# Kernel optimization log

Hardware: AMD Instinct MI355X
Metric: run time of the kernel (lower is better)

## Reference

```python
import jax, jax.numpy as jnp
import numpy as np

T, A, H, E = 16, 8, 128, 32  # steps, actions/step, hidden, embed


def setup_inputs() -> dict:
    key = jax.random.key(0)
    ks = jax.random.split(key, 16)
    n = lambda k, s: jax.random.normal(k, s, dtype=jnp.float32) * 0.1
    return {
        "old_actions": jax.random.randint(ks[0], (T,), 0, A),
        "init_input": n(ks[1], (1, E)),
        "W_ih_a": n(ks[2], (4 * H, E)), "W_hh_a": n(ks[3], (4 * H, H)),
        "b_ih_a": n(ks[4], (4 * H,)), "b_hh_a": n(ks[5], (4 * H,)),
        "heads_W": n(ks[6], (T, A, H)), "heads_b": n(ks[7], (T, A)),
        "W_ih_c": n(ks[8], (4 * H, E)), "W_hh_c": n(ks[9], (4 * H, H)),
        "b_ih_c": n(ks[10], (4 * H,)), "b_hh_c": n(ks[11], (4 * H,)),
        "critic_W": n(ks[12], (1, H)), "critic_b": n(ks[13], (1,)),
        "embed": n(ks[14], (T * A, E)),
    }


def _lstm_cell(x, h, c, W_ih, W_hh, b_ih, b_hh):
    # PyTorch LSTMCell: gate order i, f, g, o
    g = W_ih @ x + b_ih + W_hh @ h + b_hh
    i, f, gg, o = jnp.split(g, 4)
    c = jax.nn.sigmoid(f) * c + jax.nn.sigmoid(i) * jnp.tanh(gg)
    h = jax.nn.sigmoid(o) * jnp.tanh(c)
    return h, c


def reference(old_actions, init_input, W_ih_a, W_hh_a, b_ih_a, b_hh_a,
              heads_W, heads_b, W_ih_c, W_hh_c, b_ih_c, b_hh_c,
              critic_W, critic_b, embed):
    # input sequence is fully determined by the given actions
    global_idx = jnp.arange(T) * A + old_actions          # action offsets
    emb_rows = embed[global_idx]                          # [T, E]
    x_seq = jnp.concatenate([init_input, emb_rows[:-1]], axis=0)  # [T, E]

    def step(carry, xs):
        h_a, c_a, h_c, c_c = carry
        x, hw, hb, a = xs
        h_a, c_a = _lstm_cell(x, h_a, c_a, W_ih_a, W_hh_a, b_ih_a, b_hh_a)
        logits = hw @ h_a + hb                            # [A]
        logp = jax.nn.log_softmax(logits)
        probs = jnp.exp(logp)
        lp = logp[a]
        ent = -jnp.sum(probs * logp)
        h_c, c_c = _lstm_cell(x, h_c, c_c, W_ih_c, W_hh_c, b_ih_c, b_hh_c)
        val = critic_W[0] @ h_c + critic_b[0]
        return (h_a, c_a, h_c, c_c), (lp, ent, val)

    z = jnp.zeros((H,), jnp.float32)
    _, (log_probs, entropies, values) = jax.lax.scan(
        step, (z, z, z, z), (x_seq, heads_W, heads_b, old_actions))
    return log_probs, entropies, values  # each [T]
```

## Files before the change

kernel.cpp:

```cpp
#include <hip/hip_runtime.h>
#include <math.h>

#define T 16
#define A 8
#define H 128
#define E 32
#define G (4*H)

#define WS_WHH(L)   ((size_t)(L) * 131072u)
#define WS_ACCX(L)  (262144u + (size_t)(L) * 32768u)

typedef _Float16 h2t __attribute__((ext_vector_type(2)));
typedef _Float16 h8t __attribute__((ext_vector_type(8)));

__device__ __forceinline__ float sigmoidf_(float x) {
    return 1.0f / (1.0f + __expf(-x));
}
__device__ __forceinline__ float tanhf_(float x) {
    return 1.0f - 2.0f / (1.0f + __expf(2.0f * x));
}

#if __has_builtin(__builtin_amdgcn_fdot2)
#define DOT2(a, b, c) __builtin_amdgcn_fdot2((a), (b), (c), false)
#else
__device__ __forceinline__ float dot2_fb(h2t a, h2t b, float c) {
    return fmaf((float)a[0], (float)b[0], fmaf((float)a[1], (float)b[1], c));
}
#define DOT2(a, b, c) dot2_fb((a), (b), (c))
#endif

#define RPT16(M) M(0) M(1) M(2) M(3) M(4) M(5) M(6) M(7) \
                 M(8) M(9) M(10) M(11) M(12) M(13) M(14) M(15)
#define RPT8(M)  M(0) M(1) M(2) M(3) M(4) M(5) M(6) M(7)

__global__ __launch_bounds__(256)
void ppo_prep_kernel(const int* __restrict__ old_actions,
                     const float* __restrict__ init_input,
                     const float* __restrict__ W_ih_a, const float* __restrict__ W_hh_a,
                     const float* __restrict__ b_ih_a, const float* __restrict__ b_hh_a,
                     const float* __restrict__ W_ih_c, const float* __restrict__ W_hh_c,
                     const float* __restrict__ b_ih_c, const float* __restrict__ b_hh_c,
                     const float* __restrict__ embed,
                     char* __restrict__ ws)
{
    const int b = blockIdx.x;
    if (b < 64) {
        int tau  = b * 256 + threadIdx.x;
        int lstm = tau >> 13;
        int i    = tau & 8191;
        int r    = i >> 4;
        int c    = i & 15;
        const float* W = (lstm == 0) ? W_hh_a : W_hh_c;
        const float* src = W + r * H + c * 8;
        float4 fa = *(const float4*)(src);
        float4 fb = *(const float4*)(src + 4);
        h8t p = { (_Float16)fa.x, (_Float16)fa.y, (_Float16)fa.z, (_Float16)fa.w,
                  (_Float16)fb.x, (_Float16)fb.y, (_Float16)fb.z, (_Float16)fb.w };
        *(h8t*)(ws + WS_WHH(lstm) + (size_t)(c * 512 + r) * 16u) = p;
    } else {
        int tau  = (b - 64) * 256 + threadIdx.x;
        int lstm = tau >> 13;
        int i    = tau & 8191;
        int t    = i >> 9;
        int r    = i & 511;
        const float* W_ih = (lstm == 0) ? W_ih_a : W_ih_c;
        const float* b_ih = (lstm == 0) ? b_ih_a : b_ih_c;
        const float* b_hh = (lstm == 0) ? b_hh_a : b_hh_c;
        const float* xp = (t == 0) ? init_input
                                   : embed + ((t - 1) * A + old_actions[t - 1]) * E;
        const float* wr = W_ih + r * E;
        float s0 = 0.f, s1 = 0.f, s2 = 0.f, s3 = 0.f;
        #pragma unroll
        for (int e = 0; e < E; e += 4) {
            float4 wv = *(const float4*)(wr + e);
            float4 xv = *(const float4*)(xp + e);
            s0 = fmaf(wv.x, xv.x, s0); s1 = fmaf(wv.y, xv.y, s1);
            s2 = fmaf(wv.z, xv.z, s2); s3 = fmaf(wv.w, xv.w, s3);
        }
        float acc = b_ih[r] + b_hh[r] + ((s0 + s1) + (s2 + s3));
        *(float*)(ws + WS_ACCX(lstm) + (size_t)(t * 512 + r) * 4u) = acc;
    }
}

__global__ __attribute__((amdgpu_flat_work_group_size(512, 512),
                          amdgpu_waves_per_eu(2, 2)))
void ppo_ctrl_kernel(const int* __restrict__ old_actions,
                     const float* __restrict__ heads_W, const float* __restrict__ heads_b,
                     const float* __restrict__ critic_W, const float* __restrict__ critic_b,
                     const char* __restrict__ ws,
                     float* __restrict__ out)
{
    const int tid  = threadIdx.x;
    const int lane = tid & 63;
    const int wv   = tid >> 6;
    const int lstm = blockIdx.x;
    const bool actor = (lstm == 0);

    __shared__ __align__(16) float accx_lds[T * G];
    __shared__ __align__(16) float gates_s[G];
    __shared__ __align__(16) _Float16 h16[H];
    __shared__ __align__(16) _Float16 hhist[T][H];

    const float4* asrc = (const float4*)(ws + WS_ACCX(lstm));
    float4 ax0 = asrc[         tid];
    float4 ax1 = asrc[ 512 +   tid];
    float4 ax2 = asrc[1024 +   tid];
    float4 ax3 = asrc[1536 +   tid];

    const char* wbase = ws + WS_WHH(lstm);
#define LOADW(i) h8t w##i = *(const h8t*)(wbase + (size_t)((i) * 512 + tid) * 16u); \
        asm volatile("" : "+v"(w##i));
    RPT16(LOADW)
#undef LOADW

    const int tt0 = wv, tt1 = wv + 8;
#define HWLOAD(a) \
    float hl0##a = heads_W[(tt0 * A + (a)) * H + lane]; \
    float hh0##a = heads_W[(tt0 * A + (a)) * H + 64 + lane]; \
    float hl1##a = heads_W[(tt1 * A + (a)) * H + lane]; \
    float hh1##a = heads_W[(tt1 * A + (a)) * H + 64 + lane]; \
    asm volatile("" : "+v"(hl0##a), "+v"(hh0##a), "+v"(hl1##a), "+v"(hh1##a));
    RPT8(HWLOAD)
#undef HWLOAD
    float hbv0 = heads_b[tt0 * A + (lane & 7)];
    float hbv1 = heads_b[tt1 * A + (lane & 7)];
    float cw0 = critic_W[lane], cw1 = critic_W[64 + lane], cb = critic_b[0];
    int act0 = old_actions[tt0], act1 = old_actions[tt1];
    asm volatile("" : "+v"(hbv0), "+v"(hbv1), "+v"(cw0), "+v"(cw1), "+v"(cb));

    float4* adst = (float4*)accx_lds;
    adst[         tid] = ax0;
    adst[ 512 +   tid] = ax1;
    adst[1024 +   tid] = ax2;
    adst[1536 +   tid] = ax3;
    __syncthreads();

    float c_reg = 0.0f;
    const h8t* hv = (const h8t*)h16;

    #pragma unroll 1
    for (int t = 0; t < T; ++t) {
        float axv = accx_lds[t * 512 + tid];
        float a0 = 0.f, a1 = 0.f, a2 = 0.f, a3 = 0.f;
        if (t != 0) {
#define MACC(i) { h8t hq = hv[i];                                          \
            a0 = DOT2(__builtin_shufflevector(w##i, w##i, 0, 1),           \
                      __builtin_shufflevector(hq,  hq,  0, 1), a0);        \
            a1 = DOT2(__builtin_shufflevector(w##i, w##i, 2, 3),           \
                      __builtin_shufflevector(hq,  hq,  2, 3), a1);        \
            a2 = DOT2(__builtin_shufflevector(w##i, w##i, 4, 5),           \
                      __builtin_shufflevector(hq,  hq,  4, 5), a2);        \
            a3 = DOT2(__builtin_shufflevector(w##i, w##i, 6, 7),           \
                      __builtin_shufflevector(hq,  hq,  6, 7), a3); }
            RPT16(MACC)
#undef MACC
        }
        gates_s[tid] = axv + ((a0 + a1) + (a2 + a3));
        __syncthreads();

        if (tid < H) {
            float gi = gates_s[tid],       gf = gates_s[tid + H];
            float gg = gates_s[tid + 2*H], go = gates_s[tid + 3*H];
            float cn = sigmoidf_(gf) * c_reg + sigmoidf_(gi) * tanhf_(gg);
            c_reg = cn;
            float hvv = sigmoidf_(go) * tanhf_(cn);
            _Float16 hf = (_Float16)hvv;
            h16[tid] = hf;
            hhist[t][tid] = hf;
        }
        __syncthreads();
    }

    if (actor) {
#define HEADS(rep) {                                                      \
        const int tt = tt##rep;                                           \
        float hA = (float)hhist[tt][lane];                                \
        float hB = (float)hhist[tt][64 + lane];                           \
        float l0,l1,l2,l3,l4,l5,l6,l7;                                    \
        {                                                                 \
_Pragma("unroll")                                                         \
        for (int dummy = 0; dummy < 1; ++dummy) {}                        \
        }                                                                 \
        LOGIT(rep,0,l0) LOGIT(rep,1,l1) LOGIT(rep,2,l2) LOGIT(rep,3,l3)   \
        LOGIT(rep,4,l4) LOGIT(rep,5,l5) LOGIT(rep,6,l6) LOGIT(rep,7,l7)   \
        if (lane == 0) {                                                  \
            float m = fmaxf(fmaxf(fmaxf(l0, l1), fmaxf(l2, l3)),          \
                            fmaxf(fmaxf(l4, l5), fmaxf(l6, l7)));         \
            float e0 = __expf(l0 - m), e1 = __expf(l1 - m),               \
                  e2 = __expf(l2 - m), e3 = __expf(l3 - m),               \
                  e4 = __expf(l4 - m), e5 = __expf(l5 - m),               \
                  e6 = __expf(l6 - m), e7 = __expf(l7 - m);               \
            float s = ((e0 + e1) + (e2 + e3)) + ((e4 + e5) + (e6 + e7));  \
            float logZ = m + __logf(s);                                   \
            int act = act##rep;                                           \
            float la = (act == 0) ? l0 : (act == 1) ? l1 : (act == 2) ? l2 : \
                       (act == 3) ? l3 : (act == 4) ? l4 : (act == 5) ? l5 : \
                       (act == 6) ? l6 : l7;                              \
            out[tt] = la - logZ;                                          \
            float w_ = e0*(l0-logZ) + e1*(l1-logZ) + e2*(l2-logZ) + e3*(l3-logZ) \
                     + e4*(l4-logZ) + e5*(l5-logZ) + e6*(l6-logZ) + e7*(l7-logZ); \
            out[T + tt] = -w_ / s;                                        \
        } }
#define LOGIT(rep,a,dst) {                                                \
        float p = fmaf(hl##rep##a, hA, hh##rep##a * hB);                  \
        p += __shfl_xor(p, 1);  p += __shfl_xor(p, 2);                    \
        p += __shfl_xor(p, 4);  p += __shfl_xor(p, 8);                    \
        p += __shfl_xor(p, 16); p += __shfl_xor(p, 32);                   \
        dst = p + __shfl(hbv##rep, (a)); }
        HEADS(0)
        HEADS(1)
#undef LOGIT
#undef HEADS
    } else {
        #pragma unroll
        for (int rep = 0; rep < 2; ++rep) {
            const int tt = (rep == 0) ? tt0 : tt1;
            float hA = (float)hhist[tt][lane];
            float hB = (float)hhist[tt][64 + lane];
            float p = fmaf(cw0, hA, cw1 * hB);
            p += __shfl_xor(p, 1);  p += __shfl_xor(p, 2);
            p += __shfl_xor(p, 4);  p += __shfl_xor(p, 8);
            p += __shfl_xor(p, 16); p += __shfl_xor(p, 32);
            if (lane == 0) out[2 * T + tt] = p + cb;
        }
    }
}

extern "C" void kernel_launch(void* const* d_in, const int* in_sizes, int n_in,
                              void* d_out, int out_size, void* d_ws, size_t ws_size,
                              hipStream_t stream) {
    const int*   old_actions = (const int*)  d_in[0];
    const float* init_input  = (const float*)d_in[1];
    const float* W_ih_a      = (const float*)d_in[2];
    const float* W_hh_a      = (const float*)d_in[3];
    const float* b_ih_a      = (const float*)d_in[4];
    const float* b_hh_a      = (const float*)d_in[5];
    const float* heads_W     = (const float*)d_in[6];
    const float* heads_b     = (const float*)d_in[7];
    const float* W_ih_c      = (const float*)d_in[8];
    const float* W_hh_c      = (const float*)d_in[9];
    const float* b_ih_c      = (const float*)d_in[10];
    const float* b_hh_c      = (const float*)d_in[11];
    const float* critic_W    = (const float*)d_in[12];
    const float* critic_b    = (const float*)d_in[13];
    const float* embed       = (const float*)d_in[14];
    float* out = (float*)d_out;
    char* ws = (char*)d_ws;

    ppo_prep_kernel<<<dim3(128), dim3(256), 0, stream>>>(
        old_actions, init_input,
        W_ih_a, W_hh_a, b_ih_a, b_hh_a,
        W_ih_c, W_hh_c, b_ih_c, b_hh_c,
        embed, ws);

    ppo_ctrl_kernel<<<dim3(2), dim3(512), 0, stream>>>(
        old_actions, heads_W, heads_b, critic_W, critic_b, ws, out);
}
```

Measured before the change: 29.08 us.

## Fuse prep and recurrent kernels into one launch with flag-based handoff

```diff
diff --git a/kernel.cpp b/kernel.cpp
--- a/kernel.cpp
+++ b/kernel.cpp
@@ -7,8 +7,12 @@
 #define E 32
 #define G (4*H)
 
-#define WS_WHH(L)   ((size_t)(L) * 131072u)
-#define WS_ACCX(L)  (262144u + (size_t)(L) * 32768u)
+#define NPROD 32
+#define MAGIC 0x5EEDF00Du
+
+#define WS_WHH(L)    ((size_t)(L) * 131072u)
+#define WS_ACCX16(L) (262144u + (size_t)(L) * 16384u)
+#define WS_FLAGS     294912u
 
 typedef _Float16 h2t __attribute__((ext_vector_type(2)));
 typedef _Float16 h8t __attribute__((ext_vector_type(8)));
@@ -33,85 +37,76 @@
                  M(8) M(9) M(10) M(11) M(12) M(13) M(14) M(15)
 #define RPT8(M)  M(0) M(1) M(2) M(3) M(4) M(5) M(6) M(7)
 
-__global__ __launch_bounds__(256)
-void ppo_prep_kernel(const int* __restrict__ old_actions,
-                     const float* __restrict__ init_input,
-                     const float* __restrict__ W_ih_a, const float* __restrict__ W_hh_a,
-                     const float* __restrict__ b_ih_a, const float* __restrict__ b_hh_a,
-                     const float* __restrict__ W_ih_c, const float* __restrict__ W_hh_c,
-                     const float* __restrict__ b_ih_c, const float* __restrict__ b_hh_c,
-                     const float* __restrict__ embed,
-                     char* __restrict__ ws)
-{
-    const int b = blockIdx.x;
-    if (b < 64) {
-        int tau  = b * 256 + threadIdx.x;
-        int lstm = tau >> 13;
-        int i    = tau & 8191;
-        int r    = i >> 4;
-        int c    = i & 15;
-        const float* W = (lstm == 0) ? W_hh_a : W_hh_c;
-        const float* src = W + r * H + c * 8;
-        float4 fa = *(const float4*)(src);
-        float4 fb = *(const float4*)(src + 4);
-        h8t p = { (_Float16)fa.x, (_Float16)fa.y, (_Float16)fa.z, (_Float16)fa.w,
-                  (_Float16)fb.x, (_Float16)fb.y, (_Float16)fb.z, (_Float16)fb.w };
-        *(h8t*)(ws + WS_WHH(lstm) + (size_t)(c * 512 + r) * 16u) = p;
-    } else {
-        int tau  = (b - 64) * 256 + threadIdx.x;
-        int lstm = tau >> 13;
-        int i    = tau & 8191;
-        int t    = i >> 9;
-        int r    = i & 511;
-        const float* W_ih = (lstm == 0) ? W_ih_a : W_ih_c;
-        const float* b_ih = (lstm == 0) ? b_ih_a : b_ih_c;
-        const float* b_hh = (lstm == 0) ? b_hh_a : b_hh_c;
-        const float* xp = (t == 0) ? init_input
-                                   : embed + ((t - 1) * A + old_actions[t - 1]) * E;
-        const float* wr = W_ih + r * E;
-        float s0 = 0.f, s1 = 0.f, s2 = 0.f, s3 = 0.f;
-        #pragma unroll
-        for (int e = 0; e < E; e += 4) {
-            float4 wv = *(const float4*)(wr + e);
-            float4 xv = *(const float4*)(xp + e);
-            s0 = fmaf(wv.x, xv.x, s0); s1 = fmaf(wv.y, xv.y, s1);
-            s2 = fmaf(wv.z, xv.z, s2); s3 = fmaf(wv.w, xv.w, s3);
-        }
-        float acc = b_ih[r] + b_hh[r] + ((s0 + s1) + (s2 + s3));
-        *(float*)(ws + WS_ACCX(lstm) + (size_t)(t * 512 + r) * 4u) = acc;
-    }
-}
-
 __global__ __attribute__((amdgpu_flat_work_group_size(512, 512),
                           amdgpu_waves_per_eu(2, 2)))
-void ppo_ctrl_kernel(const int* __restrict__ old_actions,
-                     const float* __restrict__ heads_W, const float* __restrict__ heads_b,
-                     const float* __restrict__ critic_W, const float* __restrict__ critic_b,
-                     const char* __restrict__ ws,
-                     float* __restrict__ out)
+void ppo_fused_kernel(const int* __restrict__ old_actions,
+                      const float* __restrict__ init_input,
+                      const float* __restrict__ W_ih_a, const float* __restrict__ W_hh_a,
+                      const float* __restrict__ b_ih_a, const float* __restrict__ b_hh_a,
+                      const float* __restrict__ heads_W, const float* __restrict__ heads_b,
+                      const float* __restrict__ W_ih_c, const float* __restrict__ W_hh_c,
+                      const float* __restrict__ b_ih_c, const float* __restrict__ b_hh_c,
+                      const float* __restrict__ critic_W, const float* __restrict__ critic_b,
+                      const float* __restrict__ embed,
+                      char* __restrict__ ws,
+                      float* __restrict__ out)
 {
-    const int tid  = threadIdx.x;
+    const int tid = threadIdx.x;
+    const int b   = blockIdx.x;
+    unsigned* flags = (unsigned*)(ws + WS_FLAGS);
+
+    if (b >= 2) {
+        const int gid = (b - 2) * 512 + tid;
+        const int lstm = gid >> 13;
+        const int i    = gid & 8191;
+        {
+            const int r = i >> 4, c = i & 15;
+            const float* W = (lstm == 0) ? W_hh_a : W_hh_c;
+            const float* src = W + r * H + c * 8;
+            float4 fa = *(const float4*)(src);
+            float4 fb = *(const float4*)(src + 4);
+            h8t p = { (_Float16)fa.x, (_Float16)fa.y, (_Float16)fa.z, (_Float16)fa.w,
+                      (_Float16)fb.x, (_Float16)fb.y, (_Float16)fb.z, (_Float16)fb.w };
+            *(h8t*)(ws + WS_WHH(lstm) + (size_t)(c * 512 + r) * 16u) = p;
+        }
+        {
+            const int r = i >> 4, t = i & 15;
+            const float* W_ih = (lstm == 0) ? W_ih_a : W_ih_c;
+            const float* b_ih = (lstm == 0) ? b_ih_a : b_ih_c;
+            const float* b_hh = (lstm == 0) ? b_hh_a : b_hh_c;
+            const float* xp = (t == 0) ? init_input
+                                       : embed + ((t - 1) * A + old_actions[t - 1]) * E;
+            const float* wr = W_ih + r * E;
+            float s0 = 0.f, s1 = 0.f, s2 = 0.f, s3 = 0.f;
+            #pragma unroll
+            for (int e = 0; e < E; e += 4) {
+                float4 wv4 = *(const float4*)(wr + e);
+                float4 xv4 = *(const float4*)(xp + e);
+                s0 = fmaf(wv4.x, xv4.x, s0); s1 = fmaf(wv4.y, xv4.y, s1);
+                s2 = fmaf(wv4.z, xv4.z, s2); s3 = fmaf(wv4.w, xv4.w, s3);
+            }
+            float acc = b_ih[r] + b_hh[r] + ((s0 + s1) + (s2 + s3));
+            *(_Float16*)(ws + WS_ACCX16(lstm) + (size_t)(t * 512 + r) * 2u) = (_Float16)acc;
+        }
+        __threadfence();
+        __syncthreads();
+        if (tid == 0)
+            __hip_atomic_store(&flags[b - 2], MAGIC,
+                               __ATOMIC_RELEASE, __HIP_MEMORY_SCOPE_AGENT);
+        return;
+    }
+
     const int lane = tid & 63;
     const int wv   = tid >> 6;
-    const int lstm = blockIdx.x;
+    const int lstm = b;
     const bool actor = (lstm == 0);
 
-    __shared__ __align__(16) float accx_lds[T * G];
+    __shared__ __align__(16) _Float16 accx16[T * G];
     __shared__ __align__(16) float gates_s[G];
     __shared__ __align__(16) _Float16 h16[H];
     __shared__ __align__(16) _Float16 hhist[T][H];
 
-    const float4* asrc = (const float4*)(ws + WS_ACCX(lstm));
-    float4 ax0 = asrc[         tid];
-    float4 ax1 = asrc[ 512 +   tid];
-    float4 ax2 = asrc[1024 +   tid];
-    float4 ax3 = asrc[1536 +   tid];
-
-    const char* wbase = ws + WS_WHH(lstm);
-#define LOADW(i) h8t w##i = *(const h8t*)(wbase + (size_t)((i) * 512 + tid) * 16u); \
-        asm volatile("" : "+v"(w##i));
-    RPT16(LOADW)
-#undef LOADW
+    if (tid < H) h16[tid] = (_Float16)0.0f;
 
     const int tt0 = wv, tt1 = wv + 8;
 #define HWLOAD(a) \
@@ -128,11 +123,30 @@
     int act0 = old_actions[tt0], act1 = old_actions[tt1];
     asm volatile("" : "+v"(hbv0), "+v"(hbv1), "+v"(cw0), "+v"(cw1), "+v"(cb));
 
-    float4* adst = (float4*)accx_lds;
-    adst[         tid] = ax0;
-    adst[ 512 +   tid] = ax1;
-    adst[1024 +   tid] = ax2;
-    adst[1536 +   tid] = ax3;
+    if (wv == 0) {
+        for (;;) {
+            unsigned f = (lane < NPROD)
+                ? __hip_atomic_load(&flags[lane], __ATOMIC_ACQUIRE, __HIP_MEMORY_SCOPE_AGENT)
+                : MAGIC;
+            if (__all(f == MAGIC)) break;
+            __builtin_amdgcn_s_sleep(8);
+        }
+    }
+    __syncthreads();
+
+    const char* wbase = ws + WS_WHH(lstm);
+#define LOADW(i) h8t w##i = *(const h8t*)(wbase + (size_t)((i) * 512 + tid) * 16u); \
+        asm volatile("" : "+v"(w##i));
+    RPT16(LOADW)
+#undef LOADW
+
+    {
+        const h8t* asrc = (const h8t*)(ws + WS_ACCX16(lstm));
+        h8t aa0 = asrc[tid];
+        h8t aa1 = asrc[512 + tid];
+        ((h8t*)accx16)[tid]       = aa0;
+        ((h8t*)accx16)[512 + tid] = aa1;
+    }
     __syncthreads();
 
     float c_reg = 0.0f;
@@ -140,7 +154,7 @@
 
     #pragma unroll 1
     for (int t = 0; t < T; ++t) {
-        float axv = accx_lds[t * 512 + tid];
+        float axv = (float)accx16[t * 512 + tid];
         float a0 = 0.f, a1 = 0.f, a2 = 0.f, a3 = 0.f;
         if (t != 0) {
 #define MACC(i) { h8t hq = hv[i];                                          \
@@ -172,15 +186,17 @@
     }
 
     if (actor) {
+#define LOGIT(rep,a,dst) {                                                \
+        float p = fmaf(hl##rep##a, hA, hh##rep##a * hB);                  \
+        p += __shfl_xor(p, 1);  p += __shfl_xor(p, 2);                    \
+        p += __shfl_xor(p, 4);  p += __shfl_xor(p, 8);                    \
+        p += __shfl_xor(p, 16); p += __shfl_xor(p, 32);                   \
+        dst = p + __shfl(hbv##rep, (a)); }
 #define HEADS(rep) {                                                      \
         const int tt = tt##rep;                                           \
         float hA = (float)hhist[tt][lane];                                \
         float hB = (float)hhist[tt][64 + lane];                           \
         float l0,l1,l2,l3,l4,l5,l6,l7;                                    \
-        {                                                                 \
-_Pragma("unroll")                                                         \
-        for (int dummy = 0; dummy < 1; ++dummy) {}                        \
-        }                                                                 \
         LOGIT(rep,0,l0) LOGIT(rep,1,l1) LOGIT(rep,2,l2) LOGIT(rep,3,l3)   \
         LOGIT(rep,4,l4) LOGIT(rep,5,l5) LOGIT(rep,6,l6) LOGIT(rep,7,l7)   \
         if (lane == 0) {                                                  \
@@ -201,16 +217,10 @@
                      + e4*(l4-logZ) + e5*(l5-logZ) + e6*(l6-logZ) + e7*(l7-logZ); \
             out[T + tt] = -w_ / s;                                        \
         } }
-#define LOGIT(rep,a,dst) {                                                \
-        float p = fmaf(hl##rep##a, hA, hh##rep##a * hB);                  \
-        p += __shfl_xor(p, 1);  p += __shfl_xor(p, 2);                    \
-        p += __shfl_xor(p, 4);  p += __shfl_xor(p, 8);                    \
-        p += __shfl_xor(p, 16); p += __shfl_xor(p, 32);                   \
-        dst = p + __shfl(hbv##rep, (a)); }
         HEADS(0)
         HEADS(1)
+#undef HEADS
 #undef LOGIT
-#undef HEADS
     } else {
         #pragma unroll
         for (int rep = 0; rep < 2; ++rep) {
@@ -247,12 +257,10 @@
     float* out = (float*)d_out;
     char* ws = (char*)d_ws;
 
-    ppo_prep_kernel<<<dim3(128), dim3(256), 0, stream>>>(
+    ppo_fused_kernel<<<dim3(2 + NPROD), dim3(512), 0, stream>>>(
         old_actions, init_input,
         W_ih_a, W_hh_a, b_ih_a, b_hh_a,
+        heads_W, heads_b,
         W_ih_c, W_hh_c, b_ih_c, b_hh_c,
-        embed, ws);
-
-    ppo_ctrl_kernel<<<dim3(2), dim3(512), 0, stream>>>(
-        old_actions, heads_W, heads_b, critic_W, critic_b, ws, out);
-}
+        critic_W, critic_b, embed, ws, out);
+}
```

Result: slower. 30.18 us (+3.8%).

## Interleave gate rows so LSTM cell update uses lane shuffles, one barrier per step

Applied to the files above, without the earlier changes.

```diff
diff --git a/kernel.cpp b/kernel.cpp
--- a/kernel.cpp
+++ b/kernel.cpp
@@ -8,7 +8,7 @@
 #define G (4*H)
 
 #define WS_WHH(L)   ((size_t)(L) * 131072u)
-#define WS_ACCX(L)  (262144u + (size_t)(L) * 32768u)
+#define WS_ACCX(L)  (262144u + (size_t)(L) * 16384u)
 
 typedef _Float16 h2t __attribute__((ext_vector_type(2)));
 typedef _Float16 h8t __attribute__((ext_vector_type(8)));
@@ -48,21 +48,23 @@
         int tau  = b * 256 + threadIdx.x;
         int lstm = tau >> 13;
         int i    = tau & 8191;
-        int r    = i >> 4;
+        int k    = i >> 4;
         int c    = i & 15;
+        int r    = ((k & 3) << 7) | (k >> 2);
         const float* W = (lstm == 0) ? W_hh_a : W_hh_c;
         const float* src = W + r * H + c * 8;
         float4 fa = *(const float4*)(src);
         float4 fb = *(const float4*)(src + 4);
         h8t p = { (_Float16)fa.x, (_Float16)fa.y, (_Float16)fa.z, (_Float16)fa.w,
                   (_Float16)fb.x, (_Float16)fb.y, (_Float16)fb.z, (_Float16)fb.w };
-        *(h8t*)(ws + WS_WHH(lstm) + (size_t)(c * 512 + r) * 16u) = p;
+        *(h8t*)(ws + WS_WHH(lstm) + (size_t)(c * 512 + k) * 16u) = p;
     } else {
         int tau  = (b - 64) * 256 + threadIdx.x;
         int lstm = tau >> 13;
         int i    = tau & 8191;
         int t    = i >> 9;
-        int r    = i & 511;
+        int k    = i & 511;
+        int r    = ((k & 3) << 7) | (k >> 2);
         const float* W_ih = (lstm == 0) ? W_ih_a : W_ih_c;
         const float* b_ih = (lstm == 0) ? b_ih_a : b_ih_c;
         const float* b_hh = (lstm == 0) ? b_hh_a : b_hh_c;
@@ -78,7 +80,7 @@
             s2 = fmaf(wv.z, xv.z, s2); s3 = fmaf(wv.w, xv.w, s3);
         }
         float acc = b_ih[r] + b_hh[r] + ((s0 + s1) + (s2 + s3));
-        *(float*)(ws + WS_ACCX(lstm) + (size_t)(t * 512 + r) * 4u) = acc;
+        *(_Float16*)(ws + WS_ACCX(lstm) + (size_t)(t * 512 + k) * 2u) = (_Float16)acc;
     }
 }
 
@@ -96,16 +98,20 @@
     const int lstm = blockIdx.x;
     const bool actor = (lstm == 0);
 
-    __shared__ __align__(16) float accx_lds[T * G];
-    __shared__ __align__(16) float gates_s[G];
-    __shared__ __align__(16) _Float16 h16[H];
+    const int j = tid >> 2;
+    const int g = tid & 3;
+
+    __shared__ __align__(16) _Float16 accx16[T * 512];
+    __shared__ __align__(16) _Float16 hbuf[2][H];
     __shared__ __align__(16) _Float16 hhist[T][H];
 
-    const float4* asrc = (const float4*)(ws + WS_ACCX(lstm));
-    float4 ax0 = asrc[         tid];
-    float4 ax1 = asrc[ 512 +   tid];
-    float4 ax2 = asrc[1024 +   tid];
-    float4 ax3 = asrc[1536 +   tid];
+    {
+        const h8t* asrc = (const h8t*)(ws + WS_ACCX(lstm));
+        h8t aa0 = asrc[tid];
+        h8t aa1 = asrc[512 + tid];
+        ((h8t*)accx16)[tid]       = aa0;
+        ((h8t*)accx16)[512 + tid] = aa1;
+    }
 
     const char* wbase = ws + WS_WHH(lstm);
 #define LOADW(i) h8t w##i = *(const h8t*)(wbase + (size_t)((i) * 512 + tid) * 16u); \
@@ -128,21 +134,17 @@
     int act0 = old_actions[tt0], act1 = old_actions[tt1];
     asm volatile("" : "+v"(hbv0), "+v"(hbv1), "+v"(cw0), "+v"(cw1), "+v"(cb));
 
-    float4* adst = (float4*)accx_lds;
-    adst[         tid] = ax0;
-    adst[ 512 +   tid] = ax1;
-    adst[1024 +   tid] = ax2;
-    adst[1536 +   tid] = ax3;
     __syncthreads();
 
     float c_reg = 0.0f;
-    const h8t* hv = (const h8t*)h16;
+    const bool b0 = (g & 1) != 0, b1 = (g & 2) != 0;
 
     #pragma unroll 1
     for (int t = 0; t < T; ++t) {
-        float axv = accx_lds[t * 512 + tid];
-        float a0 = 0.f, a1 = 0.f, a2 = 0.f, a3 = 0.f;
+        float p = (float)accx16[t * 512 + tid];
         if (t != 0) {
+            const h8t* hv = (const h8t*)hbuf[t & 1];
+            float a0 = 0.f, a1 = 0.f, a2 = 0.f, a3 = 0.f;
 #define MACC(i) { h8t hq = hv[i];                                          \
             a0 = DOT2(__builtin_shufflevector(w##i, w##i, 0, 1),           \
                       __builtin_shufflevector(hq,  hq,  0, 1), a0);        \
@@ -154,33 +156,40 @@
                       __builtin_shufflevector(hq,  hq,  6, 7), a3); }
             RPT16(MACC)
 #undef MACC
-        }
-        gates_s[tid] = axv + ((a0 + a1) + (a2 + a3));
+            p += ((a0 + a1) + (a2 + a3));
+        }
+
+        float q1 = __shfl_xor(p, 1);
+        float q2 = __shfl_xor(p, 2);
+        float q3 = __shfl_xor(q1, 2);
+        float gi = b1 ? (b0 ? q3 : q2) : (b0 ? q1 : p);
+        float gf = b1 ? (b0 ? q2 : q3) : (b0 ? p  : q1);
+        float gg = b1 ? (b0 ? q1 : p ) : (b0 ? q3 : q2);
+        float go = b1 ? (b0 ? p  : q1) : (b0 ? q2 : q3);
+
+        float cn = sigmoidf_(gf) * c_reg + sigmoidf_(gi) * tanhf_(gg);
+        c_reg = cn;
+        float hvv = sigmoidf_(go) * tanhf_(cn);
+        _Float16 hf = (_Float16)hvv;
+        if (g == 0) {
+            hbuf[(t & 1) ^ 1][j] = hf;
+            hhist[t][j] = hf;
+        }
         __syncthreads();
-
-        if (tid < H) {
-            float gi = gates_s[tid],       gf = gates_s[tid + H];
-            float gg = gates_s[tid + 2*H], go = gates_s[tid + 3*H];
-            float cn = sigmoidf_(gf) * c_reg + sigmoidf_(gi) * tanhf_(gg);
-            c_reg = cn;
-            float hvv = sigmoidf_(go) * tanhf_(cn);
-            _Float16 hf = (_Float16)hvv;
-            h16[tid] = hf;
-            hhist[t][tid] = hf;
-        }
-        __syncthreads();
     }
 
     if (actor) {
+#define LOGIT(rep,a,dst) {                                                \
+        float pp = fmaf(hl##rep##a, hA, hh##rep##a * hB);                 \
+        pp += __shfl_xor(pp, 1);  pp += __shfl_xor(pp, 2);                \
+        pp += __shfl_xor(pp, 4);  pp += __shfl_xor(pp, 8);                \
+        pp += __shfl_xor(pp, 16); pp += __shfl_xor(pp, 32);               \
+        dst = pp + __shfl(hbv##rep, (a)); }
 #define HEADS(rep) {                                                      \
         const int tt = tt##rep;                                           \
         float hA = (float)hhist[tt][lane];                                \
         float hB = (float)hhist[tt][64 + lane];                           \
         float l0,l1,l2,l3,l4,l5,l6,l7;                                    \
-        {                                                                 \
-_Pragma("unroll")                                                         \
-        for (int dummy = 0; dummy < 1; ++dummy) {}                        \
-        }                                                                 \
         LOGIT(rep,0,l0) LOGIT(rep,1,l1) LOGIT(rep,2,l2) LOGIT(rep,3,l3)   \
         LOGIT(rep,4,l4) LOGIT(rep,5,l5) LOGIT(rep,6,l6) LOGIT(rep,7,l7)   \
         if (lane == 0) {                                                  \
@@ -201,16 +210,10 @@
                      + e4*(l4-logZ) + e5*(l5-logZ) + e6*(l6-logZ) + e7*(l7-logZ); \
             out[T + tt] = -w_ / s;                                        \
         } }
-#define LOGIT(rep,a,dst) {                                                \
-        float p = fmaf(hl##rep##a, hA, hh##rep##a * hB);                  \
-        p += __shfl_xor(p, 1);  p += __shfl_xor(p, 2);                    \
-        p += __shfl_xor(p, 4);  p += __shfl_xor(p, 8);                    \
-        p += __shfl_xor(p, 16); p += __shfl_xor(p, 32);                   \
-        dst = p + __shfl(hbv##rep, (a)); }
         HEADS(0)
         HEADS(1)
+#undef HEADS
 #undef LOGIT
-#undef HEADS
     } else {
         #pragma unroll
         for (int rep = 0; rep < 2; ++rep) {
```

After: 31.58 us. 1.09x slower.
